# Kernel optimization log

Hardware: AMD Instinct MI355X
Metric: run time of the kernel (lower is better)

Reference implementation:

```python
import jax, jax.numpy as jnp
import numpy as np

B, T, D, H = 32, 512, 512, 1024


def lstm_layer(x, Wx, Wh, b):
    """Standard LSTM over time. x: [B,T,in]; Wx: [in,4H]; Wh: [H,4H]; b: [4H].
    Gate order: i, f, g, o. Input projections precomputed as one batched GEMM."""
    Bsz = x.shape[0]
    Hd = Wh.shape[0]
    xg = jnp.einsum('btd,dk->btk', x, Wx) + b  # [B,T,4H]

    def step(carry, xt):
        h, c = carry
        gates = xt + h @ Wh  # [B,4H]
        i, f, g, o = jnp.split(gates, 4, axis=-1)
        c = jax.nn.sigmoid(f) * c + jax.nn.sigmoid(i) * jnp.tanh(g)
        h = jax.nn.sigmoid(o) * jnp.tanh(c)
        return (h, c), h

    h0 = jnp.zeros((Bsz, Hd), x.dtype)
    (_, _), ys = jax.lax.scan(step, (h0, h0), jnp.swapaxes(xg, 0, 1))  # ys: [T,B,H]
    return jnp.swapaxes(ys, 0, 1)  # [B,T,H]


def setup_inputs() -> dict:
    key = jax.random.key(0)
    ks = jax.random.split(key, 6)
    s_in = 1.0 / np.sqrt(D)
    s_h = 1.0 / np.sqrt(H)
    return {
        'x': jax.random.normal(ks[0], (B, T, D), jnp.float32),
        'Wx0': jax.random.normal(ks[1], (D, 4 * H), jnp.float32) * s_in,
        'Wh0': jax.random.normal(ks[2], (H, 4 * H), jnp.float32) * s_h,
        'b0': jnp.zeros((4 * H,), jnp.float32),
        'Wx1': jax.random.normal(ks[3], (H, 4 * H), jnp.float32) * s_h,
        'Wh1': jax.random.normal(ks[4], (H, 4 * H), jnp.float32) * s_h,
        'b1': jnp.zeros((4 * H,), jnp.float32),
    }


def reference(x, Wx0, Wh0, b0, Wx1, Wh1, b1):
    h = lstm_layer(x, Wx0, Wh0, b0)   # stacked layer 0
    h = lstm_layer(h, Wx1, Wh1, b1)   # stacked layer 1
    return h  # [B,T,H]
```

## Files before the change

kernel.cpp:

```cpp
#include <hip/hip_runtime.h>
#include <math.h>

#define B_  32
#define T_  512
#define D_  512
#define H_  1024
#define FH  4096
#define GRID_NB 256


__global__ void transpose_wh(const float* __restrict__ wh, float* __restrict__ wht) {
    __shared__ float tl[32][33];
    const int n0 = blockIdx.x * 32;
    const int k0 = blockIdx.y * 32;
    const int tx = threadIdx.x, ty = threadIdx.y;
#pragma unroll
    for (int j = 0; j < 4; ++j) {
        int r = ty + j * 8;
        tl[r][tx] = wh[(size_t)(k0 + r) * FH + n0 + tx];
    }
    __syncthreads();
#pragma unroll
    for (int j = 0; j < 4; ++j) {
        int r = ty + j * 8;
        wht[(size_t)(n0 + r) * H_ + k0 + tx] = tl[tx][r];
    }
}

__global__ __launch_bounds__(256) void gemm_bias_chunk(
    const float* __restrict__ A, const float* __restrict__ W,
    const float* __restrict__ bias, float* __restrict__ out, int K, int t0) {
    __shared__ float As[16 * 132];
    __shared__ float Bs[16 * 132];
    const int t  = threadIdx.x;
    const int tn = t & 15, tm = t >> 4;
    const int n0 = blockIdx.x * 128;
    const int m0 = blockIdx.y * 128;

    float acc[8][8];
#pragma unroll
    for (int i = 0; i < 8; ++i)
#pragma unroll
        for (int j = 0; j < 8; ++j) acc[i][j] = 0.f;

    for (int k0 = 0; k0 < K; k0 += 16) {
#pragma unroll
        for (int i = 0; i < 2; ++i) {
            int fid = t + i * 256;
            int m = fid >> 2, cc = fid & 3;
            int r = m0 + m;
            int arow = (r & 31) * 512 + t0 + (r >> 5);
            float4 av = *(const float4*)(A + (size_t)arow * K + k0 + cc * 4);
            As[(cc * 4 + 0) * 132 + m] = av.x;
            As[(cc * 4 + 1) * 132 + m] = av.y;
            As[(cc * 4 + 2) * 132 + m] = av.z;
            As[(cc * 4 + 3) * 132 + m] = av.w;
        }
#pragma unroll
        for (int i = 0; i < 2; ++i) {
            int fid = t + i * 256;
            int kk = fid >> 5, c = fid & 31;
            *(float4*)(Bs + kk * 132 + c * 4) =
                *(const float4*)(W + (size_t)(k0 + kk) * FH + n0 + c * 4);
        }
        __syncthreads();
#pragma unroll
        for (int kk = 0; kk < 16; ++kk) {
            float4 a0 = *(const float4*)(As + kk * 132 + tm * 8);
            float4 a1 = *(const float4*)(As + kk * 132 + tm * 8 + 4);
            float4 b0 = *(const float4*)(Bs + kk * 132 + tn * 4);
            float4 b1 = *(const float4*)(Bs + kk * 132 + 64 + tn * 4);
            float am[8] = {a0.x, a0.y, a0.z, a0.w, a1.x, a1.y, a1.z, a1.w};
            float bn[8] = {b0.x, b0.y, b0.z, b0.w, b1.x, b1.y, b1.z, b1.w};
#pragma unroll
            for (int mm = 0; mm < 8; ++mm)
#pragma unroll
                for (int nn = 0; nn < 8; ++nn) acc[mm][nn] += am[mm] * bn[nn];
        }
        __syncthreads();
    }

    float4 bb0 = *(const float4*)(bias + n0 + tn * 4);
    float4 bb1 = *(const float4*)(bias + n0 + 64 + tn * 4);
#pragma unroll
    for (int mm = 0; mm < 8; ++mm) {
        size_t orow = (size_t)(m0 + tm * 8 + mm);
        float4 v0, v1;
        v0.x = acc[mm][0] + bb0.x; v0.y = acc[mm][1] + bb0.y;
        v0.z = acc[mm][2] + bb0.z; v0.w = acc[mm][3] + bb0.w;
        v1.x = acc[mm][4] + bb1.x; v1.y = acc[mm][5] + bb1.y;
        v1.z = acc[mm][6] + bb1.z; v1.w = acc[mm][7] + bb1.w;
        *(float4*)(out + orow * FH + n0 + tn * 4)      = v0;
        *(float4*)(out + orow * FH + n0 + 64 + tn * 4) = v1;
    }
}

__device__ __forceinline__ float4 ldg_cg4(const float* p) {
    float4 r;
    asm volatile("global_load_dwordx4 %0, %1, off sc0 sc1" : "=v"(r) : "v"(p));
    return r;
}
__device__ __forceinline__ float ldg_cg1(const float* p) {
    float r;
    asm volatile("global_load_dword %0, %1, off sc0 sc1" : "=v"(r) : "v"(p));
    return r;
}
__device__ __forceinline__ void stg_cg1(float* p, float v) {
    asm volatile("global_store_dword %0, %1, off sc0 sc1" :: "v"(p), "v"(v));
}
#define WAITVM(n) asm volatile("s_waitcnt vmcnt(" #n ")" ::: "memory")

__device__ __forceinline__ void grid_barrier(unsigned* bar, unsigned k) {
    WAITVM(0);
    __syncthreads();
    if (threadIdx.x == 0) {
        unsigned* gen = bar;
        unsigned* l2  = bar + 32;
        unsigned* l1  = bar + 64 + (blockIdx.x & 15u) * 32u;
        if (__hip_atomic_fetch_add(l1, 1u, __ATOMIC_RELAXED,
                                   __HIP_MEMORY_SCOPE_AGENT) == k * 16u + 15u) {
            if (__hip_atomic_fetch_add(l2, 1u, __ATOMIC_RELAXED,
                                       __HIP_MEMORY_SCOPE_AGENT) == k * 16u + 15u) {
                __hip_atomic_store(gen, k + 1u, __ATOMIC_RELAXED,
                                   __HIP_MEMORY_SCOPE_AGENT);
            }
        }
        while (__hip_atomic_load(gen, __ATOMIC_RELAXED,
                                 __HIP_MEMORY_SCOPE_AGENT) < k + 1u)
            __builtin_amdgcn_s_sleep(2);
    }
    __syncthreads();
}

__global__ __launch_bounds__(512, 2) void lstm_seq(
    const float* __restrict__ wht,
    const float* __restrict__ xgc,
    float* __restrict__ hb0,
    float* __restrict__ hb1,
    float* __restrict__ cbuf,
    float* __restrict__ out,
    unsigned* __restrict__ bar,
    int t0, int Tc, int gbase)
{
    __shared__ __align__(16) float smem[17408];
    float4* hsA4 = (float4*)smem;
    float4* hsB4 = hsA4 + 1024;

    const int t   = threadIdx.x;
    const int q   = t >> 8;
    const int u   = t & 255;
    const int hc0 = blockIdx.x * 4;

    const int gcg = u & 1;
    const int sl  = (u >> 1) & 31;
    const int bg  = u >> 6;

    const float4* wt4 = (const float4*)wht;
    int wr0, wr1, wr2, wr3;
    {
        int r0 = gcg * 4;
        wr0 = (((r0 + 0) >> 1) * H_ + hc0 + q * 2 + ((r0 + 0) & 1)) * 256;
        wr1 = (((r0 + 1) >> 1) * H_ + hc0 + q * 2 + ((r0 + 1) & 1)) * 256;
        wr2 = (((r0 + 2) >> 1) * H_ + hc0 + q * 2 + ((r0 + 2) & 1)) * 256;
        wr3 = (((r0 + 3) >> 1) * H_ + hc0 + q * 2 + ((r0 + 3) & 1)) * 256;
    }
#define DECLW(ch) \
    float4 w##ch##0 = wt4[wr0 + (ch) * 32 + sl]; \
    float4 w##ch##1 = wt4[wr1 + (ch) * 32 + sl]; \
    float4 w##ch##2 = wt4[wr2 + (ch) * 32 + sl]; \
    float4 w##ch##3 = wt4[wr3 + (ch) * 32 + sl];
    DECLW(0) DECLW(1) DECLW(2) DECLW(3) DECLW(4) DECLW(5) DECLW(6) DECLW(7)

    float creg = 0.f;
    if (u < 64) creg = cbuf[(size_t)(u >> 1) * H_ + hc0 + q * 2 + (u & 1)];

    const int hoff0 = (t >> 5) * H_ + (t & 31) * 4;
    const int hoff1 = hoff0 + 16 * H_;
    float* scq = smem + q * 8448;
    float* g4q = smem + 16896 + q * 256;

    for (int tt = t0; tt < t0 + Tc; ++tt) {
        const float* hp = (tt & 1) ? hb1 : hb0;
        float* hn       = (tt & 1) ? hb0 : hb1;
        const float* xg_t = xgc + (size_t)(tt - t0) * (B_ * FH);

        float xgv = ldg_cg1(xg_t + (size_t)((u >> 1) & 31) * FH +
                            (u >> 6) * H_ + hc0 + q * 2 + (u & 1));

        float acc[4][8];
#pragma unroll
        for (int i = 0; i < 4; ++i)
#pragma unroll
            for (int j = 0; j < 8; ++j) acc[i][j] = 0.f;

        float4 ra0, ra1, ra2, ra3, ra4, ra5, ra6, ra7;
        float4 rb0, rb1, rb2, rb3, rb4, rb5, rb6, rb7;
#define ISSUE(ch) do { \
        ra##ch = ldg_cg4(hp + hoff0 + (ch) * 128); \
        rb##ch = ldg_cg4(hp + hoff1 + (ch) * 128); } while (0)
#define WRITEC(ch, base) do { \
        (base)[t]       = ra##ch; \
        (base)[t + 512] = rb##ch; } while (0)
#define FMA4(a, wv, hv) a += wv.x*hv.x + wv.y*hv.y + wv.z*hv.z + wv.w*hv.w
#define COMPUTE(ch, base) do { \
        const float4* hbp = (const float4*)(base); \
        _Pragma("unroll") \
        for (int bi = 0; bi < 8; ++bi) { \
            float4 hv = hbp[(bg * 8 + bi) * 32 + sl]; \
            FMA4(acc[0][bi], w##ch##0, hv); \
            FMA4(acc[1][bi], w##ch##1, hv); \
            FMA4(acc[2][bi], w##ch##2, hv); \
            FMA4(acc[3][bi], w##ch##3, hv); \
        } } while (0)

        ISSUE(0); ISSUE(1); ISSUE(2); ISSUE(3);
        WAITVM(6); WRITEC(0, hsA4);
        __syncthreads();
        ISSUE(4); WAITVM(6); WRITEC(1, hsB4); COMPUTE(0, hsA4); __syncthreads();
        ISSUE(5); WAITVM(6); WRITEC(2, hsA4); COMPUTE(1, hsB4); __syncthreads();
        ISSUE(6); WAITVM(6); WRITEC(3, hsB4); COMPUTE(2, hsA4); __syncthreads();
        ISSUE(7); WAITVM(6); WRITEC(4, hsA4); COMPUTE(3, hsB4); __syncthreads();
        WAITVM(4); WRITEC(5, hsB4); COMPUTE(4, hsA4); __syncthreads();
        WAITVM(2); WRITEC(6, hsA4); COMPUTE(5, hsB4); __syncthreads();
        WAITVM(0); WRITEC(7, hsB4); COMPUTE(6, hsA4); __syncthreads();
        COMPUTE(7, hsB4);
        __syncthreads();

#pragma unroll
        for (int gi = 0; gi < 4; ++gi)
#pragma unroll
            for (int bi = 0; bi < 8; ++bi)
                scq[((gcg * 4 + gi) * 32 + bg * 8 + bi) * 33 + sl] = acc[gi][bi];
        __syncthreads();

        {
            int hcl = u & 1, b = (u >> 1) & 31, gt = u >> 6;
            int r = gt * 2 + hcl;
            float s = 0.f;
#pragma unroll
            for (int j = 0; j < 32; ++j) s += scq[(r * 32 + b) * 33 + j];
            g4q[gt * 64 + (u & 63)] = s + xgv;
        }
        __syncthreads();

        if (u < 64) {
            int hcl = u & 1, b = u >> 1;
            int hc = hc0 + q * 2 + hcl;
            float vi = g4q[u], vf = g4q[64 + u], vg = g4q[128 + u], vo = g4q[192 + u];
            float si = 1.f / (1.f + __expf(-vi));
            float sf = 1.f / (1.f + __expf(-vf));
            float so = 1.f / (1.f + __expf(-vo));
            float tg = tanhf(vg);
            float cn = sf * creg + si * tg;
            creg = cn;
            float hv = so * tanhf(cn);
            stg_cg1(hn + (size_t)b * H_ + hc, hv);
            out[(size_t)b * (T_ * H_) + (size_t)tt * H_ + hc] = hv;
        }

        if (tt != t0 + Tc - 1)
            grid_barrier(bar, (unsigned)(gbase + (tt - t0)));
    }

    if (u < 64)
        cbuf[(size_t)(u >> 1) * H_ + hc0 + q * 2 + (u & 1)] = creg;
}

extern "C" void kernel_launch(void* const* d_in, const int* in_sizes, int n_in,
                              void* d_out, int out_size, void* d_ws, size_t ws_size,
                              hipStream_t stream) {
    (void)in_sizes; (void)n_in; (void)out_size;
    const float* x   = (const float*)d_in[0];
    const float* Wx0 = (const float*)d_in[1];
    const float* Wh0 = (const float*)d_in[2];
    const float* b0  = (const float*)d_in[3];
    const float* Wx1 = (const float*)d_in[4];
    const float* Wh1 = (const float*)d_in[5];
    const float* b1  = (const float*)d_in[6];
    float* out = (float*)d_out;

    char* ws = (char*)d_ws;
    float* wht  = (float*)(ws);
    float* hb0  = (float*)(ws + 16777216ull);
    float* hb1  = hb0 + 32 * 1024;
    float* cbuf = hb1 + 32 * 1024;
    unsigned* bar = (unsigned*)(ws + 17170432ull);
    float* xgc  = (float*)(ws + 17174528ull);

    const size_t base = 17174528ull;
    int Tc;
    if      (ws_size >= base + 512ull * 524288ull) Tc = 512;
    else if (ws_size >= base +  64ull * 524288ull) Tc = 64;
    else if (ws_size >= base +  16ull * 524288ull) Tc = 16;
    else                                           Tc = 4;

    hipMemsetAsync(bar, 0, 4096, stream);
    int gb = 0;

    for (int layer = 0; layer < 2; ++layer) {
        const float* Aptr = layer ? out : x;
        const float* Wxp  = layer ? Wx1 : Wx0;
        const float* Whp  = layer ? Wh1 : Wh0;
        const float* bp   = layer ? b1  : b0;
        const int    K    = layer ? H_  : D_;

        transpose_wh<<<dim3(128, 32), dim3(32, 8), 0, stream>>>(Whp, wht);
        hipMemsetAsync(hb0, 0, 131072, stream);
        hipMemsetAsync(cbuf, 0, 131072, stream);

        for (int t0 = 0; t0 < T_; t0 += Tc) {
            gemm_bias_chunk<<<dim3(32, Tc / 4), 256, 0, stream>>>(
                Aptr, Wxp, bp, xgc, K, t0);

            const float* a0 = wht; const float* a1 = xgc;
            float* a2 = hb0; float* a3 = hb1; float* a4 = cbuf; float* a5 = out;
            unsigned* a6 = bar; int a7 = t0; int a8 = Tc; int a9 = gb;
            void* kargs[] = {&a0, &a1, &a2, &a3, &a4, &a5, &a6, &a7, &a8, &a9};
            hipLaunchCooperativeKernel(lstm_seq, dim3(GRID_NB), dim3(512),
                                       kargs, 0, stream);
            gb += Tc - 1;
        }
    }
}
```

Before: 12.18 ms.

## Stage recurrent weight slice in LDS instead of registers, shrink h prefetch ring

Each block's slice of the transposed Wh moves from 128 persistent VGPRs per thread into padded LDS, loaded once at kernel start, and is re-read from LDS in every compute chunk. The in-flight h prefetch drops from eight register pairs to a three-slot rotating ring, and the xg/c loads lose their cache-bypass hints. The aim is to relieve register pressure, since launch bounds ask for 512 threads with 2 blocks per CU. In exchange LDS use roughly doubles to about 135KB, which may itself cap residency, and each step adds extra LDS weight reads.

```diff
diff --git a/kernel.cpp b/kernel.cpp
--- a/kernel.cpp
+++ b/kernel.cpp
@@ -100,9 +100,9 @@
     asm volatile("global_load_dwordx4 %0, %1, off sc0 sc1" : "=v"(r) : "v"(p));
     return r;
 }
-__device__ __forceinline__ float ldg_cg1(const float* p) {
+__device__ __forceinline__ float ldg_pl1(const float* p) {
     float r;
-    asm volatile("global_load_dword %0, %1, off sc0 sc1" : "=v"(r) : "v"(p));
+    asm volatile("global_load_dword %0, %1, off" : "=v"(r) : "v"(p));
     return r;
 }
 __device__ __forceinline__ void stg_cg1(float* p, float v) {
@@ -142,9 +142,10 @@
     unsigned* __restrict__ bar,
     int t0, int Tc, int gbase)
 {
-    __shared__ __align__(16) float smem[17408];
-    float4* hsA4 = (float4*)smem;
-    float4* hsB4 = hsA4 + 1024;
+    __shared__ __align__(16) float smem[33856];
+    float4* whs4  = (float4*)smem;
+    float4* bufA4 = (float4*)(smem + 16448);
+    float4* bufB4 = bufA4 + 1024;
 
     const int t   = threadIdx.x;
     const int q   = t >> 8;
@@ -155,37 +156,40 @@
     const int sl  = (u >> 1) & 31;
     const int bg  = u >> 6;
 
-    const float4* wt4 = (const float4*)wht;
-    int wr0, wr1, wr2, wr3;
     {
-        int r0 = gcg * 4;
-        wr0 = (((r0 + 0) >> 1) * H_ + hc0 + q * 2 + ((r0 + 0) & 1)) * 256;
-        wr1 = (((r0 + 1) >> 1) * H_ + hc0 + q * 2 + ((r0 + 1) & 1)) * 256;
-        wr2 = (((r0 + 2) >> 1) * H_ + hc0 + q * 2 + ((r0 + 2) & 1)) * 256;
-        wr3 = (((r0 + 3) >> 1) * H_ + hc0 + q * 2 + ((r0 + 3) & 1)) * 256;
-    }
-#define DECLW(ch) \
-    float4 w##ch##0 = wt4[wr0 + (ch) * 32 + sl]; \
-    float4 w##ch##1 = wt4[wr1 + (ch) * 32 + sl]; \
-    float4 w##ch##2 = wt4[wr2 + (ch) * 32 + sl]; \
-    float4 w##ch##3 = wt4[wr3 + (ch) * 32 + sl];
-    DECLW(0) DECLW(1) DECLW(2) DECLW(3) DECLW(4) DECLW(5) DECLW(6) DECLW(7)
-
-    float creg = 0.f;
-    if (u < 64) creg = cbuf[(size_t)(u >> 1) * H_ + hc0 + q * 2 + (u & 1)];
-
-    const int hoff0 = (t >> 5) * H_ + (t & 31) * 4;
-    const int hoff1 = hoff0 + 16 * H_;
-    float* scq = smem + q * 8448;
-    float* g4q = smem + 16896 + q * 256;
+        const float4* wht4 = (const float4*)wht;
+#pragma unroll
+        for (int i = 0; i < 8; ++i) {
+            int fid = t + i * 512;
+            int r = fid >> 8, cc = fid & 255;
+            int gate = (r & 7) >> 1;
+            int col  = hc0 + (r >> 3) * 2 + (r & 1);
+            whs4[r * 257 + cc] = wht4[(size_t)(gate * H_ + col) * 256 + cc];
+        }
+    }
+
+    float creg = ldg_pl1(cbuf + (size_t)((u & 63) >> 1) * H_ + hc0 + q * 2 + (u & 1));
+    WAITVM(0);
+    if (u >= 64) creg = 0.f;
+    __syncthreads();
+
+    const int wrow0 = (q * 8 + gcg * 4 + 0) * 257;
+    const int wrow1 = (q * 8 + gcg * 4 + 1) * 257;
+    const int wrow2 = (q * 8 + gcg * 4 + 2) * 257;
+    const int wrow3 = (q * 8 + gcg * 4 + 3) * 257;
+    const size_t xgoff = (size_t)((u >> 1) & 31) * FH + (u >> 6) * H_ + hc0 + q * 2 + (u & 1);
+    float* scq = smem + 16448 + q * 8448;
+    float* g4q = smem + 33344 + q * 256;
 
     for (int tt = t0; tt < t0 + Tc; ++tt) {
         const float* hp = (tt & 1) ? hb1 : hb0;
         float* hn       = (tt & 1) ? hb0 : hb1;
         const float* xg_t = xgc + (size_t)(tt - t0) * (B_ * FH);
 
-        float xgv = ldg_cg1(xg_t + (size_t)((u >> 1) & 31) * FH +
-                            (u >> 6) * H_ + hc0 + q * 2 + (u & 1));
+        const float* p0 = hp + (t >> 5) * H_ + (t & 31) * 4;
+        const float* p1 = p0 + 16 * H_;
+
+        float xgv = ldg_pl1(xg_t + xgoff);
 
         float acc[4][8];
 #pragma unroll
@@ -193,38 +197,41 @@
 #pragma unroll
             for (int j = 0; j < 8; ++j) acc[i][j] = 0.f;
 
-        float4 ra0, ra1, ra2, ra3, ra4, ra5, ra6, ra7;
-        float4 rb0, rb1, rb2, rb3, rb4, rb5, rb6, rb7;
-#define ISSUE(ch) do { \
-        ra##ch = ldg_cg4(hp + hoff0 + (ch) * 128); \
-        rb##ch = ldg_cg4(hp + hoff1 + (ch) * 128); } while (0)
-#define WRITEC(ch, base) do { \
-        (base)[t]       = ra##ch; \
-        (base)[t + 512] = rb##ch; } while (0)
-#define FMA4(a, wv, hv) a += wv.x*hv.x + wv.y*hv.y + wv.z*hv.z + wv.w*hv.w
-#define COMPUTE(ch, base) do { \
-        const float4* hbp = (const float4*)(base); \
+        float4 rgA0, rgA1, rgB0, rgB1, rgC0, rgC1;
+
+#define ISSUE(S, ch) do { \
+        rg##S##0 = ldg_cg4(p0 + (ch) * 128); \
+        rg##S##1 = ldg_cg4(p1 + (ch) * 128); } while (0)
+#define WRITEC(S, buf) do { (buf)[t] = rg##S##0; (buf)[t + 512] = rg##S##1; } while (0)
+#define COMPUTE(ch, buf) do { \
+        float4 w0 = whs4[wrow0 + (ch) * 32 + sl]; \
+        float4 w1 = whs4[wrow1 + (ch) * 32 + sl]; \
+        float4 w2 = whs4[wrow2 + (ch) * 32 + sl]; \
+        float4 w3 = whs4[wrow3 + (ch) * 32 + sl]; \
+        const float4* hbp = (const float4*)(buf); \
         _Pragma("unroll") \
         for (int bi = 0; bi < 8; ++bi) { \
             float4 hv = hbp[(bg * 8 + bi) * 32 + sl]; \
-            FMA4(acc[0][bi], w##ch##0, hv); \
-            FMA4(acc[1][bi], w##ch##1, hv); \
-            FMA4(acc[2][bi], w##ch##2, hv); \
-            FMA4(acc[3][bi], w##ch##3, hv); \
+            acc[0][bi] += w0.x*hv.x + w0.y*hv.y + w0.z*hv.z + w0.w*hv.w; \
+            acc[1][bi] += w1.x*hv.x + w1.y*hv.y + w1.z*hv.z + w1.w*hv.w; \
+            acc[2][bi] += w2.x*hv.x + w2.y*hv.y + w2.z*hv.z + w2.w*hv.w; \
+            acc[3][bi] += w3.x*hv.x + w3.y*hv.y + w3.z*hv.z + w3.w*hv.w; \
         } } while (0)
 
-        ISSUE(0); ISSUE(1); ISSUE(2); ISSUE(3);
-        WAITVM(6); WRITEC(0, hsA4);
-        __syncthreads();
-        ISSUE(4); WAITVM(6); WRITEC(1, hsB4); COMPUTE(0, hsA4); __syncthreads();
-        ISSUE(5); WAITVM(6); WRITEC(2, hsA4); COMPUTE(1, hsB4); __syncthreads();
-        ISSUE(6); WAITVM(6); WRITEC(3, hsB4); COMPUTE(2, hsA4); __syncthreads();
-        ISSUE(7); WAITVM(6); WRITEC(4, hsA4); COMPUTE(3, hsB4); __syncthreads();
-        WAITVM(4); WRITEC(5, hsB4); COMPUTE(4, hsA4); __syncthreads();
-        WAITVM(2); WRITEC(6, hsA4); COMPUTE(5, hsB4); __syncthreads();
-        WAITVM(0); WRITEC(7, hsB4); COMPUTE(6, hsA4); __syncthreads();
-        COMPUTE(7, hsB4);
-        __syncthreads();
+        ISSUE(A, 0); ISSUE(B, 1); ISSUE(C, 2);
+        WAITVM(4); WRITEC(A, bufA4); __syncthreads();
+        ISSUE(A, 3); WAITVM(4); WRITEC(B, bufB4); COMPUTE(0, bufA4); __syncthreads();
+        ISSUE(B, 4); WAITVM(4); WRITEC(C, bufA4); COMPUTE(1, bufB4); __syncthreads();
+        ISSUE(C, 5); WAITVM(4); WRITEC(A, bufB4); COMPUTE(2, bufA4); __syncthreads();
+        ISSUE(A, 6); WAITVM(4); WRITEC(B, bufA4); COMPUTE(3, bufB4); __syncthreads();
+        ISSUE(B, 7); WAITVM(4); WRITEC(C, bufB4); COMPUTE(4, bufA4); __syncthreads();
+        WAITVM(2); WRITEC(A, bufA4); COMPUTE(5, bufB4); __syncthreads();
+        WAITVM(0); WRITEC(B, bufB4); COMPUTE(6, bufA4); __syncthreads();
+        COMPUTE(7, bufB4);
+        __syncthreads();
+#undef ISSUE
+#undef WRITEC
+#undef COMPUTE
 
 #pragma unroll
         for (int gi = 0; gi < 4; ++gi)
@@ -260,6 +267,8 @@
 
         if (tt != t0 + Tc - 1)
             grid_barrier(bar, (unsigned)(gbase + (tt - t0)));
+        else
+            __syncthreads();
     }
 
     if (u < 64)
```

New measurement: 12.84 ms. 1.05x slower.
